# Kernel optimization log

Measured on AMD Instinct MI355X. Metric: run time of the kernel, lower is better.

The kernel has to match this reference:

```python
import jax, jax.numpy as jnp
import numpy as np

N_NODES = 100000
N_EDGES = 6400000


def gcn_conv(x, edge_index, edge_weight, W, b):
    """PyG GCNConv: add self-loops (weight 1), symmetric deg^{-1/2} normalization,
    linear transform, edge-weighted scatter-add aggregation, then bias."""
    n = x.shape[0]
    row, col = edge_index[0], edge_index[1]  # source, target
    # add self loops
    loop = jnp.arange(n, dtype=edge_index.dtype)
    row = jnp.concatenate([row, loop])
    col = jnp.concatenate([col, loop])
    w = jnp.concatenate([edge_weight, jnp.ones((n,), dtype=edge_weight.dtype)])
    # symmetric normalization: deg computed on target index
    deg = jax.ops.segment_sum(w, col, num_segments=n)
    dinv = jnp.where(deg > 0, jax.lax.rsqrt(deg), 0.0)
    norm = dinv[row] * w * dinv[col]  # [E+N]
    # transform then gather/scatter (transform first: smaller feature dim is fine either way)
    h = x @ W  # [N, F_out]
    msg = norm[:, None] * h[row]  # [E+N, F_out]
    out = jax.ops.segment_sum(msg, col, num_segments=n)
    return out + b


def setup_inputs() -> dict:
    key = jax.random.key(0)
    k1, k2, k3, k4, k5, k6 = jax.random.split(key, 6)
    x = jax.random.normal(k1, (N_NODES, 16), dtype=jnp.float32)
    edge_index = jax.random.randint(k2, (2, N_EDGES), 0, N_NODES, dtype=jnp.int64)
    edge_weight = jax.random.uniform(k3, (N_EDGES,), dtype=jnp.float32)
    # glorot-style init for GCN weights
    W1 = jax.random.normal(k4, (16, 8), dtype=jnp.float32) * (1.0 / np.sqrt(16))
    b1 = jnp.zeros((8,), dtype=jnp.float32)
    W2 = jax.random.normal(k5, (8, 2), dtype=jnp.float32) * (1.0 / np.sqrt(8))
    b2 = jnp.zeros((2,), dtype=jnp.float32)
    return {"x": x, "edge_index": edge_index, "edge_weight": edge_weight,
            "W1": W1, "b1": b1, "W2": W2, "b2": b2}


def reference(x, edge_index, edge_weight, W1, b1, W2, b2):
    x_emb = gcn_conv(x, edge_index, edge_weight, W1, b1)
    h = jax.nn.relu(x_emb)
    # F.dropout(training=self.training) is identity in eval mode
    out = gcn_conv(h, edge_index, edge_weight, W2, b2)
    return (out, x_emb)
```

## Files before the change

### kernel.cpp

```cpp
#include <hip/hip_runtime.h>


#define NN 100000
#define NE 6400000

#define GROUPS 50
#define GSIZE  2000
#define CAP    140000
#define BK     2048
#define NBB    (NE/BK)


__device__ __forceinline__ void atomAdd(float* p, float v) {
#if defined(__HIP_DEVICE_COMPILE__)
    unsafeAtomicAdd(p, v);
#else
    atomicAdd(p, v);
#endif
}

__device__ __forceinline__ void load4(const void* __restrict__ ei, int is64, size_t q,
                                      size_t halfoff, int v[4]) {
    if (is64) {
        const longlong2* p = (const longlong2*)((const long long*)ei + halfoff);
        longlong2 a = p[2 * q], b = p[2 * q + 1];
        v[0] = (int)a.x; v[1] = (int)a.y; v[2] = (int)b.x; v[3] = (int)b.y;
    } else {
        int4 t = ((const int4*)((const int*)ei + halfoff))[q];
        v[0] = t.x; v[1] = t.y; v[2] = t.z; v[3] = t.w;
    }
}

__global__ void k_detect(const int* __restrict__ ei32, int* __restrict__ flag) {
    int z = 0;
#pragma unroll
    for (int i = 1; i < 64; i += 2) z |= ei32[i];
    *flag = (z == 0) ? 1 : 0;
}


__global__ __launch_bounds__(256) void k_bucket(const void* __restrict__ ei,
                                                const float* __restrict__ ew,
                                                const int* __restrict__ flag,
                                                unsigned* __restrict__ cursors,
                                                unsigned long long* __restrict__ buckets) {
    __shared__ int hist[GROUPS];
    __shared__ int base[GROUPS];
    const int is64 = *flag;
    const int t = threadIdx.x;
    if (t < GROUPS) hist[t] = 0;
    __syncthreads();
    const size_t q0 = (size_t)blockIdx.x * (BK / 4);
#pragma unroll
    for (int it = 0; it < BK / 4 / 256; ++it) {
        size_t q = q0 + (size_t)it * 256 + t;
        int c[4]; load4(ei, is64, q, NE, c);
#pragma unroll
        for (int k = 0; k < 4; ++k) atomicAdd(&hist[c[k] / GSIZE], 1);
    }
    __syncthreads();
    if (t < GROUPS) {
        base[t] = (int)atomicAdd(&cursors[t], (unsigned)hist[t]);
        hist[t] = 0;
    }
    __syncthreads();
#pragma unroll
    for (int it = 0; it < BK / 4 / 256; ++it) {
        size_t q = q0 + (size_t)it * 256 + t;
        int r[4], c[4];
        load4(ei, is64, q, 0, r);
        load4(ei, is64, q, NE, c);
        float4 wv = ((const float4*)ew)[q];
        float w[4] = {wv.x, wv.y, wv.z, wv.w};
#pragma unroll
        for (int k = 0; k < 4; ++k) {
            int g = c[k] / GSIZE;
            int cl = c[k] - g * GSIZE;
            int idx = atomicAdd(&hist[g], 1) + base[g];
            if (idx < CAP) {
                unsigned pk = (unsigned)r[k] | ((unsigned)cl << 17);
                buckets[(size_t)g * CAP + idx] =
                    (unsigned long long)pk | ((unsigned long long)__float_as_uint(w[k]) << 32);
            }
        }
    }
}

__global__ __launch_bounds__(512) void k_deg(const unsigned* __restrict__ cursors,
                                             const unsigned long long* __restrict__ buckets,
                                             int kch,
                                             float* __restrict__ degpart) {
    __shared__ float acc[GSIZE];
    const int t = threadIdx.x;
    const int g = blockIdx.x / kch, j = blockIdx.x % kch;
    for (int i = t; i < GSIZE; i += 512) acc[i] = 0.0f;
    __syncthreads();
    unsigned cu = cursors[g];
    const int cnt = (int)(cu < (unsigned)CAP ? cu : (unsigned)CAP);
    const int cpk = (cnt + kch - 1) / kch;
    const int lo = j * cpk;
    const int hi = (lo + cpk < cnt) ? lo + cpk : cnt;
    const unsigned long long* B = buckets + (size_t)g * CAP;
    for (int i = lo + t; i < hi; i += 512) {
        unsigned long long rec = B[i];
        int cl = ((unsigned)rec) >> 17;
        float w = __uint_as_float((unsigned)(rec >> 32));
        atomicAdd(&acc[cl], w);
    }
    __syncthreads();
    float* dst = degpart + ((size_t)g * kch + j) * GSIZE;
    for (int i = t; i < GSIZE; i += 512) dst[i] = acc[i];
}

template <int KCH>
__global__ __launch_bounds__(256) void k_node1m(const float* __restrict__ x,
                                                const float* __restrict__ W1,
                                                const float* __restrict__ degpart,
                                                float* __restrict__ dinv,
                                                float* __restrict__ h1s) {
    __shared__ float sW[128];
    if (threadIdx.x < 128) sW[threadIdx.x] = W1[threadIdx.x];
    __syncthreads();
    int i = blockIdx.x * blockDim.x + threadIdx.x;
    if (i >= NN) return;
    int g = i / GSIZE, il = i - g * GSIZE;
    float d = 1.0f;
#pragma unroll
    for (int j = 0; j < KCH; ++j) d += degpart[((size_t)g * KCH + j) * GSIZE + il];
    float di = rsqrtf(d);
    dinv[i] = di;
    const float4* xp = reinterpret_cast<const float4*>(x + (size_t)i * 16);
    float acc[8];
#pragma unroll
    for (int j = 0; j < 8; ++j) acc[j] = 0.0f;
#pragma unroll
    for (int kq = 0; kq < 4; ++kq) {
        float4 v = xp[kq];
        float vv[4] = {v.x, v.y, v.z, v.w};
#pragma unroll
        for (int kk = 0; kk < 4; ++kk) {
            int k = kq * 4 + kk;
#pragma unroll
            for (int j = 0; j < 8; ++j) acc[j] += vv[kk] * sW[k * 8 + j];
        }
    }
    float4* hp = reinterpret_cast<float4*>(h1s + (size_t)i * 8);
    hp[0] = make_float4(di * acc[0], di * acc[1], di * acc[2], di * acc[3]);
    hp[1] = make_float4(di * acc[4], di * acc[5], di * acc[6], di * acc[7]);
}

__global__ __launch_bounds__(512) void k_gather1(const unsigned* __restrict__ cursors,
                                                 const unsigned long long* __restrict__ buckets,
                                                 int kch,
                                                 const float* __restrict__ h1s,
                                                 float* __restrict__ g1part) {
    __shared__ float acc[GSIZE * 8];
    const int t = threadIdx.x;
    const int g = blockIdx.x / kch, j = blockIdx.x % kch;
    for (int i = t; i < GSIZE * 8; i += 512) acc[i] = 0.0f;
    __syncthreads();
    unsigned cu = cursors[g];
    const int cnt = (int)(cu < (unsigned)CAP ? cu : (unsigned)CAP);
    const int cpk = (cnt + kch - 1) / kch;
    const int lo = j * cpk;
    const int hi = (lo + cpk < cnt) ? lo + cpk : cnt;
    const unsigned long long* B = buckets + (size_t)g * CAP;
    for (int i = lo + t; i < hi; i += 512) {
        unsigned long long rec = B[i];
        unsigned pk = (unsigned)rec;
        int r = pk & 0x1FFFF;
        int cl = pk >> 17;
        float w = __uint_as_float((unsigned)(rec >> 32));
        const float4* hp = (const float4*)(h1s + (size_t)r * 8);
        float4 a = hp[0], b = hp[1];
        float* A = acc + cl * 8;
        atomicAdd(A + 0, w * a.x);
        atomicAdd(A + 1, w * a.y);
        atomicAdd(A + 2, w * a.z);
        atomicAdd(A + 3, w * a.w);
        atomicAdd(A + 4, w * b.x);
        atomicAdd(A + 5, w * b.y);
        atomicAdd(A + 6, w * b.z);
        atomicAdd(A + 7, w * b.w);
    }
    __syncthreads();
    float* dst = g1part + ((size_t)g * kch + j) * (GSIZE * 8);
    for (int i = t; i < GSIZE * 8; i += 512) dst[i] = acc[i];
}

template <int KCH>
__global__ __launch_bounds__(256) void k_epi1m(const float* __restrict__ g1part,
                                               const float* __restrict__ h1s,
                                               const float* __restrict__ dinv,
                                               const float* __restrict__ W2,
                                               const float* __restrict__ b1,
                                               float* __restrict__ xemb,
                                               float* __restrict__ h2s) {
    int i = blockIdx.x * blockDim.x + threadIdx.x;
    if (i >= NN) return;
    int g = i / GSIZE, il = i - g * GSIZE;
    float s[8];
#pragma unroll
    for (int m = 0; m < 8; ++m) s[m] = 0.0f;
#pragma unroll
    for (int j = 0; j < KCH; ++j) {
        const float4* p = (const float4*)(g1part + (((size_t)g * KCH + j) * GSIZE + il) * 8);
        float4 a = p[0], b = p[1];
        s[0] += a.x; s[1] += a.y; s[2] += a.z; s[3] += a.w;
        s[4] += b.x; s[5] += b.y; s[6] += b.z; s[7] += b.w;
    }
    float di = dinv[i];
    const float4* hp = (const float4*)(h1s + (size_t)i * 8);
    float4 ha = hp[0], hb = hp[1];
    float hv[8] = {ha.x, ha.y, ha.z, ha.w, hb.x, hb.y, hb.z, hb.w};
    float e[8];
#pragma unroll
    for (int m = 0; m < 8; ++m) e[m] = di * (s[m] + hv[m]) + b1[m];
    float4* xo = reinterpret_cast<float4*>(xemb + (size_t)i * 8);
    xo[0] = make_float4(e[0], e[1], e[2], e[3]);
    xo[1] = make_float4(e[4], e[5], e[6], e[7]);
    float s0 = 0.0f, s1 = 0.0f;
#pragma unroll
    for (int m = 0; m < 8; ++m) {
        float rr = fmaxf(e[m], 0.0f);
        s0 += rr * W2[m * 2 + 0];
        s1 += rr * W2[m * 2 + 1];
    }
    *reinterpret_cast<float2*>(h2s + (size_t)i * 2) = make_float2(di * s0, di * s1);
}

__global__ __launch_bounds__(512) void k_gather2(const unsigned* __restrict__ cursors,
                                                 const unsigned long long* __restrict__ buckets,
                                                 int kch,
                                                 const float* __restrict__ h2s,
                                                 float* __restrict__ g2part) {
    __shared__ float acc[GSIZE * 2];
    const int t = threadIdx.x;
    const int g = blockIdx.x / kch, j = blockIdx.x % kch;
    for (int i = t; i < GSIZE * 2; i += 512) acc[i] = 0.0f;
    __syncthreads();
    unsigned cu = cursors[g];
    const int cnt = (int)(cu < (unsigned)CAP ? cu : (unsigned)CAP);
    const int cpk = (cnt + kch - 1) / kch;
    const int lo = j * cpk;
    const int hi = (lo + cpk < cnt) ? lo + cpk : cnt;
    const unsigned long long* B = buckets + (size_t)g * CAP;
    for (int i = lo + t; i < hi; i += 512) {
        unsigned long long rec = B[i];
        unsigned pk = (unsigned)rec;
        int r = pk & 0x1FFFF;
        int cl = pk >> 17;
        float w = __uint_as_float((unsigned)(rec >> 32));
        float2 v = *(const float2*)(h2s + (size_t)r * 2);
        atomicAdd(&acc[cl * 2 + 0], w * v.x);
        atomicAdd(&acc[cl * 2 + 1], w * v.y);
    }
    __syncthreads();
    float* dst = g2part + ((size_t)g * kch + j) * (GSIZE * 2);
    for (int i = t; i < GSIZE * 2; i += 512) dst[i] = acc[i];
}

template <int KCH>
__global__ __launch_bounds__(256) void k_epi2m(const float* __restrict__ g2part,
                                               const float* __restrict__ h2s,
                                               const float* __restrict__ dinv,
                                               const float* __restrict__ b2,
                                               float* __restrict__ out) {
    int i = blockIdx.x * blockDim.x + threadIdx.x;
    if (i >= NN) return;
    int g = i / GSIZE, il = i - g * GSIZE;
    float s0 = 0.0f, s1 = 0.0f;
#pragma unroll
    for (int j = 0; j < KCH; ++j) {
        float2 p = *(const float2*)(g2part + (((size_t)g * KCH + j) * GSIZE + il) * 2);
        s0 += p.x; s1 += p.y;
    }
    float di = dinv[i];
    float2 h = *(const float2*)(h2s + (size_t)i * 2);
    *reinterpret_cast<float2*>(out + (size_t)i * 2) =
        make_float2(di * (s0 + h.x) + b2[0], di * (s1 + h.y) + b2[1]);
}


__global__ __launch_bounds__(256) void k_prep(const void* __restrict__ ei,
                                              const float* __restrict__ ew,
                                              const int* __restrict__ flag,
                                              float* __restrict__ deg) {
    const int is64 = *flag;
    const int stride = gridDim.x * blockDim.x;
    const int nv = NE / 4;
    const float4* ewv = (const float4*)ew;
    for (int v = blockIdx.x * blockDim.x + threadIdx.x; v < nv; v += stride) {
        int c[4]; load4(ei, is64, v, NE, c);
        float4 w = ewv[v];
        atomAdd(&deg[c[0]], w.x);
        atomAdd(&deg[c[1]], w.y);
        atomAdd(&deg[c[2]], w.z);
        atomAdd(&deg[c[3]], w.w);
    }
}

__global__ __launch_bounds__(256) void k_node1(const float* __restrict__ x,
                                               const float* __restrict__ W1,
                                               const float* __restrict__ deg,
                                               float* __restrict__ dinv,
                                               float* __restrict__ h1) {
    __shared__ float sW[128];
    if (threadIdx.x < 128) sW[threadIdx.x] = W1[threadIdx.x];
    __syncthreads();
    int i = blockIdx.x * blockDim.x + threadIdx.x;
    if (i >= NN) return;
    float d = deg[i] + 1.0f;
    dinv[i] = rsqrtf(d);
    const float4* xp = reinterpret_cast<const float4*>(x + (size_t)i * 16);
    float acc[8];
#pragma unroll
    for (int j = 0; j < 8; ++j) acc[j] = 0.0f;
#pragma unroll
    for (int kq = 0; kq < 4; ++kq) {
        float4 v = xp[kq];
        float vv[4] = {v.x, v.y, v.z, v.w};
#pragma unroll
        for (int kk = 0; kk < 4; ++kk) {
            int k = kq * 4 + kk;
#pragma unroll
            for (int j = 0; j < 8; ++j) acc[j] += vv[kk] * sW[k * 8 + j];
        }
    }
    float4* hp = reinterpret_cast<float4*>(h1 + (size_t)i * 8);
    hp[0] = make_float4(acc[0], acc[1], acc[2], acc[3]);
    hp[1] = make_float4(acc[4], acc[5], acc[6], acc[7]);
}

__device__ __forceinline__ void agg1_edge(int r, int c, float w,
                                          const float* __restrict__ dinv,
                                          const float* __restrict__ h1,
                                          float* __restrict__ agg1) {
    float nrm = dinv[r] * w * dinv[c];
    const float4* hp = reinterpret_cast<const float4*>(h1 + (size_t)r * 8);
    float4 a = hp[0];
    float4 b = hp[1];
    float* o = agg1 + (size_t)c * 8;
    atomAdd(o + 0, nrm * a.x);
    atomAdd(o + 1, nrm * a.y);
    atomAdd(o + 2, nrm * a.z);
    atomAdd(o + 3, nrm * a.w);
    atomAdd(o + 4, nrm * b.x);
    atomAdd(o + 5, nrm * b.y);
    atomAdd(o + 6, nrm * b.z);
    atomAdd(o + 7, nrm * b.w);
}

__global__ __launch_bounds__(256) void k_agg1(const void* __restrict__ ei,
                                              const float* __restrict__ ew,
                                              const int* __restrict__ flag,
                                              const float* __restrict__ dinv,
                                              const float* __restrict__ h1,
                                              float* __restrict__ agg1) {
    const int is64 = *flag;
    const int stride = gridDim.x * blockDim.x;
    const int nv = NE / 4;
    const float4* ewv = (const float4*)ew;
    for (int v = blockIdx.x * blockDim.x + threadIdx.x; v < nv; v += stride) {
        int r[4], c[4];
        load4(ei, is64, v, 0, r);
        load4(ei, is64, v, NE, c);
        float4 w = ewv[v];
        agg1_edge(r[0], c[0], w.x, dinv, h1, agg1);
        agg1_edge(r[1], c[1], w.y, dinv, h1, agg1);
        agg1_edge(r[2], c[2], w.z, dinv, h1, agg1);
        agg1_edge(r[3], c[3], w.w, dinv, h1, agg1);
    }
}

__global__ __launch_bounds__(256) void k_epi1(const float* __restrict__ agg1,
                                              const float* __restrict__ h1,
                                              const float* __restrict__ dinv,
                                              const float* __restrict__ W2,
                                              const float* __restrict__ b1,
                                              float* __restrict__ xemb,
                                              float* __restrict__ h2) {
    int i = blockIdx.x * blockDim.x + threadIdx.x;
    if (i >= NN) return;
    float di = dinv[i];
    float d2 = di * di;
    const float4* ap = reinterpret_cast<const float4*>(agg1 + (size_t)i * 8);
    const float4* hp = reinterpret_cast<const float4*>(h1 + (size_t)i * 8);
    float4 a0 = ap[0], a1 = ap[1];
    float4 g0 = hp[0], g1 = hp[1];
    float e[8];
    e[0] = a0.x + d2 * g0.x + b1[0];
    e[1] = a0.y + d2 * g0.y + b1[1];
    e[2] = a0.z + d2 * g0.z + b1[2];
    e[3] = a0.w + d2 * g0.w + b1[3];
    e[4] = a1.x + d2 * g1.x + b1[4];
    e[5] = a1.y + d2 * g1.y + b1[5];
    e[6] = a1.z + d2 * g1.z + b1[6];
    e[7] = a1.w + d2 * g1.w + b1[7];
    float4* xo = reinterpret_cast<float4*>(xemb + (size_t)i * 8);
    xo[0] = make_float4(e[0], e[1], e[2], e[3]);
    xo[1] = make_float4(e[4], e[5], e[6], e[7]);
    float s0 = 0.0f, s1 = 0.0f;
#pragma unroll
    for (int j = 0; j < 8; ++j) {
        float r = fmaxf(e[j], 0.0f);
        s0 += r * W2[j * 2 + 0];
        s1 += r * W2[j * 2 + 1];
    }
    *reinterpret_cast<float2*>(h2 + (size_t)i * 2) = make_float2(s0, s1);
}

__device__ __forceinline__ void agg2_edge(int r, int c, float w,
                                          const float* __restrict__ dinv,
                                          const float* __restrict__ h2,
                                          float* __restrict__ agg2) {
    float nrm = dinv[r] * w * dinv[c];
    float2 v = *reinterpret_cast<const float2*>(h2 + (size_t)r * 2);
    float* o = agg2 + (size_t)c * 2;
    atomAdd(o + 0, nrm * v.x);
    atomAdd(o + 1, nrm * v.y);
}

__global__ __launch_bounds__(256) void k_agg2(const void* __restrict__ ei,
                                              const float* __restrict__ ew,
                                              const int* __restrict__ flag,
                                              const float* __restrict__ dinv,
                                              const float* __restrict__ h2,
                                              float* __restrict__ agg2) {
    const int is64 = *flag;
    const int stride = gridDim.x * blockDim.x;
    const int nv = NE / 4;
    const float4* ewv = (const float4*)ew;
    for (int v = blockIdx.x * blockDim.x + threadIdx.x; v < nv; v += stride) {
        int r[4], c[4];
        load4(ei, is64, v, 0, r);
        load4(ei, is64, v, NE, c);
        float4 w = ewv[v];
        agg2_edge(r[0], c[0], w.x, dinv, h2, agg2);
        agg2_edge(r[1], c[1], w.y, dinv, h2, agg2);
        agg2_edge(r[2], c[2], w.z, dinv, h2, agg2);
        agg2_edge(r[3], c[3], w.w, dinv, h2, agg2);
    }
}

__global__ __launch_bounds__(256) void k_epi2(const float* __restrict__ agg2,
                                              const float* __restrict__ h2,
                                              const float* __restrict__ dinv,
                                              const float* __restrict__ b2,
                                              float* __restrict__ out) {
    int i = blockIdx.x * blockDim.x + threadIdx.x;
    if (i >= NN) return;
    float di = dinv[i];
    float d2 = di * di;
    float2 a = *reinterpret_cast<const float2*>(agg2 + (size_t)i * 2);
    float2 h = *reinterpret_cast<const float2*>(h2 + (size_t)i * 2);
    *reinterpret_cast<float2*>(out + (size_t)i * 2) =
        make_float2(a.x + d2 * h.x + b2[0], a.y + d2 * h.y + b2[1]);
}


extern "C" void kernel_launch(void* const* d_in, const int* in_sizes, int n_in,
                              void* d_out, int out_size, void* d_ws, size_t ws_size,
                              hipStream_t stream) {
    const float* x  = (const float*)d_in[0];
    const void*  ei = d_in[1];
    const float* ew = (const float*)d_in[2];
    const float* W1 = (const float*)d_in[3];
    const float* b1 = (const float*)d_in[4];
    const float* W2 = (const float*)d_in[5];
    const float* b2 = (const float*)d_in[6];

    float* out  = (float*)d_out;
    float* xemb = out + (size_t)NN * 2;

    const int NB = (NN + 255) / 256;

    size_t o_buckets, o_g1, o_g2, o_deg, o_h1, o_h2, o_dinv, o_cur, o_flag, need;
    auto plan = [&](int kc) {
        size_t p = 0;
        o_buckets = p; p += (size_t)GROUPS * CAP * 8;
        o_g1   = p; p += (size_t)GROUPS * kc * GSIZE * 8 * 4;
        o_g2   = p; p += (size_t)GROUPS * kc * GSIZE * 2 * 4;
        o_deg  = p; p += (size_t)GROUPS * kc * GSIZE * 4;
        o_h1   = p; p += (size_t)NN * 8 * 4;
        o_h2   = p; p += (size_t)NN * 2 * 4;
        o_dinv = p; p += (size_t)NN * 4;
        o_cur  = p; p += GROUPS * 4;
        o_flag = p; p += 16;
        need = p;
    };

    int kch = 0;
    plan(10); if (ws_size >= need) kch = 10;
    if (!kch) { plan(6); if (ws_size >= need) kch = 6; }

    char* ws = (char*)d_ws;

    if (kch) {
        unsigned long long* buckets = (unsigned long long*)(ws + o_buckets);
        float* g1part  = (float*)(ws + o_g1);
        float* g2part  = (float*)(ws + o_g2);
        float* degpart = (float*)(ws + o_deg);
        float* h1s     = (float*)(ws + o_h1);
        float* h2s     = (float*)(ws + o_h2);
        float* dinv    = (float*)(ws + o_dinv);
        unsigned* cursors = (unsigned*)(ws + o_cur);
        int* flag      = (int*)(ws + o_flag);

        hipMemsetAsync(cursors, 0, GROUPS * 4, stream);

        k_detect <<<1, 1, 0, stream>>>((const int*)ei, flag);
        k_bucket <<<NBB, 256, 0, stream>>>(ei, ew, flag, cursors, buckets);
        k_deg    <<<GROUPS * kch, 512, 0, stream>>>(cursors, buckets, kch, degpart);
        if (kch == 10) k_node1m<10><<<NB, 256, 0, stream>>>(x, W1, degpart, dinv, h1s);
        else           k_node1m<6> <<<NB, 256, 0, stream>>>(x, W1, degpart, dinv, h1s);
        k_gather1<<<GROUPS * kch, 512, 0, stream>>>(cursors, buckets, kch, h1s, g1part);
        if (kch == 10) k_epi1m<10><<<NB, 256, 0, stream>>>(g1part, h1s, dinv, W2, b1, xemb, h2s);
        else           k_epi1m<6> <<<NB, 256, 0, stream>>>(g1part, h1s, dinv, W2, b1, xemb, h2s);
        k_gather2<<<GROUPS * kch, 512, 0, stream>>>(cursors, buckets, kch, h2s, g2part);
        if (kch == 10) k_epi2m<10><<<NB, 256, 0, stream>>>(g2part, h2s, dinv, b2, out);
        else           k_epi2m<6> <<<NB, 256, 0, stream>>>(g2part, h2s, dinv, b2, out);
    } else {
        float* deg  = (float*)d_ws;
        float* agg1 = deg + NN;
        float* agg2 = agg1 + (size_t)NN * 8;
        float* dinv = agg2 + (size_t)NN * 2;
        float* h1   = dinv + NN;
        float* h2   = h1 + (size_t)NN * 8;
        int*   flag = (int*)(h2 + (size_t)NN * 2);

        hipMemsetAsync(deg, 0, (size_t)NN * (1 + 8 + 2) * sizeof(float), stream);

        const int EB = 2048;
        k_detect<<<1, 1, 0, stream>>>((const int*)ei, flag);
        k_prep <<<EB, 256, 0, stream>>>(ei, ew, flag, deg);
        k_node1<<<NB, 256, 0, stream>>>(x, W1, deg, dinv, h1);
        k_agg1 <<<EB, 256, 0, stream>>>(ei, ew, flag, dinv, h1, agg1);
        k_epi1 <<<NB, 256, 0, stream>>>(agg1, h1, dinv, W2, b1, xemb, h2);
        k_agg2 <<<EB, 256, 0, stream>>>(ei, ew, flag, dinv, h2, agg2);
        k_epi2 <<<NB, 256, 0, stream>>>(agg2, h2, dinv, b2, out);
    }
}
```

Measured before the change: 568.1 us.

## Halve bucket group size and map gather threads to feature lanes

Buckets now cover 1000 target nodes each (100 groups), with a fixed 6-way chunk split, so there are 600 blocks per pass and less LDS per block (32KB accumulator). The gather kernels assign one feature component per thread (8 or 2 threads per edge), giving coalesced reads of h rows and one LDS atomic per thread instead of eight or two. The cost is that each edge record is read by 8 (or 2) threads, and the 10-chunk workspace path is removed. Bucket overflow risk changes because CAP scales with group size, so the margin over the mean edges per group is the same proportion.

```diff
diff --git a/kernel.cpp b/kernel.cpp
--- a/kernel.cpp
+++ b/kernel.cpp
@@ -4,9 +4,10 @@
 #define NN 100000
 #define NE 6400000
 
-#define GROUPS 50
-#define GSIZE  2000
-#define CAP    140000
+#define GROUPS 100
+#define GSIZE  1000
+#define KCH    6
+#define CAP    70000
 #define BK     2048
 #define NBB    (NE/BK)
 
@@ -88,16 +89,15 @@
 
 __global__ __launch_bounds__(512) void k_deg(const unsigned* __restrict__ cursors,
                                              const unsigned long long* __restrict__ buckets,
-                                             int kch,
                                              float* __restrict__ degpart) {
     __shared__ float acc[GSIZE];
     const int t = threadIdx.x;
-    const int g = blockIdx.x / kch, j = blockIdx.x % kch;
+    const int g = blockIdx.x / KCH, j = blockIdx.x % KCH;
     for (int i = t; i < GSIZE; i += 512) acc[i] = 0.0f;
     __syncthreads();
     unsigned cu = cursors[g];
     const int cnt = (int)(cu < (unsigned)CAP ? cu : (unsigned)CAP);
-    const int cpk = (cnt + kch - 1) / kch;
+    const int cpk = (cnt + KCH - 1) / KCH;
     const int lo = j * cpk;
     const int hi = (lo + cpk < cnt) ? lo + cpk : cnt;
     const unsigned long long* B = buckets + (size_t)g * CAP;
@@ -108,11 +108,10 @@
         atomicAdd(&acc[cl], w);
     }
     __syncthreads();
-    float* dst = degpart + ((size_t)g * kch + j) * GSIZE;
+    float* dst = degpart + ((size_t)g * KCH + j) * GSIZE;
     for (int i = t; i < GSIZE; i += 512) dst[i] = acc[i];
 }
 
-template <int KCH>
 __global__ __launch_bounds__(256) void k_node1m(const float* __restrict__ x,
                                                 const float* __restrict__ W1,
                                                 const float* __restrict__ degpart,
@@ -151,44 +150,35 @@
 
 __global__ __launch_bounds__(512) void k_gather1(const unsigned* __restrict__ cursors,
                                                  const unsigned long long* __restrict__ buckets,
-                                                 int kch,
                                                  const float* __restrict__ h1s,
                                                  float* __restrict__ g1part) {
     __shared__ float acc[GSIZE * 8];
     const int t = threadIdx.x;
-    const int g = blockIdx.x / kch, j = blockIdx.x % kch;
+    const int g = blockIdx.x / KCH, j = blockIdx.x % KCH;
     for (int i = t; i < GSIZE * 8; i += 512) acc[i] = 0.0f;
     __syncthreads();
     unsigned cu = cursors[g];
     const int cnt = (int)(cu < (unsigned)CAP ? cu : (unsigned)CAP);
-    const int cpk = (cnt + kch - 1) / kch;
+    const int cpk = (cnt + KCH - 1) / KCH;
     const int lo = j * cpk;
     const int hi = (lo + cpk < cnt) ? lo + cpk : cnt;
     const unsigned long long* B = buckets + (size_t)g * CAP;
-    for (int i = lo + t; i < hi; i += 512) {
+    const int k = t & 7;
+    const int rs = t >> 3;
+    for (int i = lo + rs; i < hi; i += 64) {
         unsigned long long rec = B[i];
         unsigned pk = (unsigned)rec;
         int r = pk & 0x1FFFF;
         int cl = pk >> 17;
         float w = __uint_as_float((unsigned)(rec >> 32));
-        const float4* hp = (const float4*)(h1s + (size_t)r * 8);
-        float4 a = hp[0], b = hp[1];
-        float* A = acc + cl * 8;
-        atomicAdd(A + 0, w * a.x);
-        atomicAdd(A + 1, w * a.y);
-        atomicAdd(A + 2, w * a.z);
-        atomicAdd(A + 3, w * a.w);
-        atomicAdd(A + 4, w * b.x);
-        atomicAdd(A + 5, w * b.y);
-        atomicAdd(A + 6, w * b.z);
-        atomicAdd(A + 7, w * b.w);
-    }
-    __syncthreads();
-    float* dst = g1part + ((size_t)g * kch + j) * (GSIZE * 8);
+        float h = h1s[(size_t)r * 8 + k];
+        atomicAdd(&acc[cl * 8 + k], w * h);
+    }
+    __syncthreads();
+    float* dst = g1part + ((size_t)g * KCH + j) * (GSIZE * 8);
     for (int i = t; i < GSIZE * 8; i += 512) dst[i] = acc[i];
 }
 
-template <int KCH>
 __global__ __launch_bounds__(256) void k_epi1m(const float* __restrict__ g1part,
                                                const float* __restrict__ h1s,
                                                const float* __restrict__ dinv,
@@ -231,36 +221,35 @@
 
 __global__ __launch_bounds__(512) void k_gather2(const unsigned* __restrict__ cursors,
                                                  const unsigned long long* __restrict__ buckets,
-                                                 int kch,
                                                  const float* __restrict__ h2s,
                                                  float* __restrict__ g2part) {
     __shared__ float acc[GSIZE * 2];
     const int t = threadIdx.x;
-    const int g = blockIdx.x / kch, j = blockIdx.x % kch;
+    const int g = blockIdx.x / KCH, j = blockIdx.x % KCH;
     for (int i = t; i < GSIZE * 2; i += 512) acc[i] = 0.0f;
     __syncthreads();
     unsigned cu = cursors[g];
     const int cnt = (int)(cu < (unsigned)CAP ? cu : (unsigned)CAP);
-    const int cpk = (cnt + kch - 1) / kch;
+    const int cpk = (cnt + KCH - 1) / KCH;
     const int lo = j * cpk;
     const int hi = (lo + cpk < cnt) ? lo + cpk : cnt;
     const unsigned long long* B = buckets + (size_t)g * CAP;
-    for (int i = lo + t; i < hi; i += 512) {
+    const int k = t & 1;
+    const int rs = t >> 1;
+    for (int i = lo + rs; i < hi; i += 256) {
         unsigned long long rec = B[i];
         unsigned pk = (unsigned)rec;
         int r = pk & 0x1FFFF;
         int cl = pk >> 17;
         float w = __uint_as_float((unsigned)(rec >> 32));
-        float2 v = *(const float2*)(h2s + (size_t)r * 2);
-        atomicAdd(&acc[cl * 2 + 0], w * v.x);
-        atomicAdd(&acc[cl * 2 + 1], w * v.y);
-    }
-    __syncthreads();
-    float* dst = g2part + ((size_t)g * kch + j) * (GSIZE * 2);
+        float h = h2s[(size_t)r * 2 + k];
+        atomicAdd(&acc[cl * 2 + k], w * h);
+    }
+    __syncthreads();
+    float* dst = g2part + ((size_t)g * KCH + j) * (GSIZE * 2);
     for (int i = t; i < GSIZE * 2; i += 512) dst[i] = acc[i];
 }
 
-template <int KCH>
 __global__ __launch_bounds__(256) void k_epi2m(const float* __restrict__ g2part,
                                                const float* __restrict__ h2s,
                                                const float* __restrict__ dinv,
@@ -475,28 +464,21 @@
 
     const int NB = (NN + 255) / 256;
 
-    size_t o_buckets, o_g1, o_g2, o_deg, o_h1, o_h2, o_dinv, o_cur, o_flag, need;
-    auto plan = [&](int kc) {
-        size_t p = 0;
-        o_buckets = p; p += (size_t)GROUPS * CAP * 8;
-        o_g1   = p; p += (size_t)GROUPS * kc * GSIZE * 8 * 4;
-        o_g2   = p; p += (size_t)GROUPS * kc * GSIZE * 2 * 4;
-        o_deg  = p; p += (size_t)GROUPS * kc * GSIZE * 4;
-        o_h1   = p; p += (size_t)NN * 8 * 4;
-        o_h2   = p; p += (size_t)NN * 2 * 4;
-        o_dinv = p; p += (size_t)NN * 4;
-        o_cur  = p; p += GROUPS * 4;
-        o_flag = p; p += 16;
-        need = p;
-    };
-
-    int kch = 0;
-    plan(10); if (ws_size >= need) kch = 10;
-    if (!kch) { plan(6); if (ws_size >= need) kch = 6; }
+    size_t p = 0;
+    size_t o_buckets = p; p += (size_t)GROUPS * CAP * 8;
+    size_t o_g1   = p; p += (size_t)GROUPS * KCH * GSIZE * 8 * 4;
+    size_t o_g2   = p; p += (size_t)GROUPS * KCH * GSIZE * 2 * 4;
+    size_t o_deg  = p; p += (size_t)GROUPS * KCH * GSIZE * 4;
+    size_t o_h1   = p; p += (size_t)NN * 8 * 4;
+    size_t o_h2   = p; p += (size_t)NN * 2 * 4;
+    size_t o_dinv = p; p += (size_t)NN * 4;
+    size_t o_cur  = p; p += GROUPS * 4;
+    size_t o_flag = p; p += 16;
+    const size_t need = p;
 
     char* ws = (char*)d_ws;
 
-    if (kch) {
+    if (ws_size >= need) {
         unsigned long long* buckets = (unsigned long long*)(ws + o_buckets);
         float* g1part  = (float*)(ws + o_g1);
         float* g2part  = (float*)(ws + o_g2);
@@ -511,15 +493,12 @@
 
         k_detect <<<1, 1, 0, stream>>>((const int*)ei, flag);
         k_bucket <<<NBB, 256, 0, stream>>>(ei, ew, flag, cursors, buckets);
-        k_deg    <<<GROUPS * kch, 512, 0, stream>>>(cursors, buckets, kch, degpart);
-        if (kch == 10) k_node1m<10><<<NB, 256, 0, stream>>>(x, W1, degpart, dinv, h1s);
-        else           k_node1m<6> <<<NB, 256, 0, stream>>>(x, W1, degpart, dinv, h1s);
-        k_gather1<<<GROUPS * kch, 512, 0, stream>>>(cursors, buckets, kch, h1s, g1part);
-        if (kch == 10) k_epi1m<10><<<NB, 256, 0, stream>>>(g1part, h1s, dinv, W2, b1, xemb, h2s);
-        else           k_epi1m<6> <<<NB, 256, 0, stream>>>(g1part, h1s, dinv, W2, b1, xemb, h2s);
-        k_gather2<<<GROUPS * kch, 512, 0, stream>>>(cursors, buckets, kch, h2s, g2part);
-        if (kch == 10) k_epi2m<10><<<NB, 256, 0, stream>>>(g2part, h2s, dinv, b2, out);
-        else           k_epi2m<6> <<<NB, 256, 0, stream>>>(g2part, h2s, dinv, b2, out);
+        k_deg    <<<GROUPS * KCH, 512, 0, stream>>>(cursors, buckets, degpart);
+        k_node1m <<<NB, 256, 0, stream>>>(x, W1, degpart, dinv, h1s);
+        k_gather1<<<GROUPS * KCH, 512, 0, stream>>>(cursors, buckets, h1s, g1part);
+        k_epi1m  <<<NB, 256, 0, stream>>>(g1part, h1s, dinv, W2, b1, xemb, h2s);
+        k_gather2<<<GROUPS * KCH, 512, 0, stream>>>(cursors, buckets, h2s, g2part);
+        k_epi2m  <<<NB, 256, 0, stream>>>(g2part, h2s, dinv, b2, out);
     } else {
         float* deg  = (float*)d_ws;
         float* agg1 = deg + NN;
```

Result: slower. 672.3 us (+18.3%).
